# Performance work log

Hardware: AMD Instinct MI355X
Metric: run time of the kernel (lower is better)

## Reference

```python
import jax, jax.numpy as jnp
import numpy as np
from jax import lax

EPS = 1e-8


def setup_inputs() -> dict:
    key = jax.random.key(0)
    k1, k2, k3, k4, k5 = jax.random.split(key, 5)
    b, c_in, c_out, h, w_sp, k, z = 8, 256, 256, 128, 128, 3, 512
    return {
        "x": jax.random.normal(k1, (b, c_in, h, w_sp), dtype=jnp.float32),
        "w": jax.random.normal(k2, (b, z), dtype=jnp.float32),
        "weight": jax.random.normal(k3, (c_out, c_in, k, k), dtype=jnp.float32),
        "affine_w": jax.random.normal(k4, (c_in, z), dtype=jnp.float32) * 0.02,
        "affine_b": jax.random.normal(k5, (c_in,), dtype=jnp.float32) * 0.02,
    }


def reference(x, w, weight, affine_w, affine_b):
    # style: [b, c_in] -> broadcast over (out_ch, kh, kw); +1 as in StyleGAN2
    style = w @ affine_w.T + affine_b + 1.0                      # [b, c_in]
    wgt = weight[None] * style[:, None, :, None, None]           # [b, O, I, kh, kw]
    # demodulation
    denom = lax.rsqrt(jnp.sum(wgt * wgt, axis=(2, 3, 4)) + EPS)  # [b, O]
    wgt = wgt * denom[:, :, None, None, None]

    # per-sample conv (equivalent to groups=b grouped conv), 'same' padding
    def conv_one(xi, wi):
        # xi: [I, H, W], wi: [O, I, kh, kw]
        return lax.conv_general_dilated(
            xi[None], wi, window_strides=(1, 1), padding="SAME",
            dimension_numbers=("NCHW", "OIHW", "NCHW"))[0]

    return jax.vmap(conv_one)(x, wgt)                            # [b, O, H, W]
```

## Files before the change

kernel.cpp:

```cpp
#include <hip/hip_runtime.h>

#define EPS 1e-8f

using short8 = __attribute__((ext_vector_type(8))) short;
using f32x16 = __attribute__((ext_vector_type(16))) float;
typedef unsigned short u16;

#define WAITV(N) asm volatile("s_waitcnt vmcnt(" #N ")" ::: "memory")
#define BARRIER() do { __builtin_amdgcn_s_barrier(); \
                       asm volatile("" ::: "memory"); } while (0)

__device__ __forceinline__ u16 f2bf(float f) {
    union { float f; unsigned u; } v; v.f = f;
    unsigned u = v.u;
    return (u16)((u + 0x7FFFu + ((u >> 16) & 1u)) >> 16);
}

__device__ __forceinline__ void g2l16(const void* gsrc, void* ldst) {
    __builtin_amdgcn_global_load_lds(
        (const __attribute__((address_space(1))) unsigned int*)gsrc,
        (__attribute__((address_space(3))) unsigned int*)ldst, 16, 0, 0);
}

__global__ void style_kernel(const float* __restrict__ w,
                             const float* __restrict__ affine_w,
                             const float* __restrict__ affine_b,
                             float* __restrict__ style) {
    int b = blockIdx.x;
    int i = threadIdx.x;
    __shared__ float wb[512];
    for (int z = threadIdx.x; z < 512; z += 256) wb[z] = w[b * 512 + z];
    __syncthreads();
    const float* aw = affine_w + i * 512;
    float acc = 0.f;
#pragma unroll 4
    for (int z = 0; z < 512; z += 4) {
        float4 a4 = *reinterpret_cast<const float4*>(aw + z);
        acc += a4.x * wb[z] + a4.y * wb[z + 1] + a4.z * wb[z + 2] + a4.w * wb[z + 3];
    }
    style[b * 256 + i] = acc + affine_b[i] + 1.0f;
}

__global__ void modw_kernel(const float* __restrict__ weight,
                            const float* __restrict__ style,
                            u16* __restrict__ wgt) {
    int b = blockIdx.x >> 8;
    int o = blockIdx.x & 255;
    int ic = threadIdx.x;
    float s = style[b * 256 + ic];
    const float* wp = weight + (size_t)(o * 256 + ic) * 9;
    float m[9];
    float ss = 0.f;
#pragma unroll
    for (int t = 0; t < 9; ++t) { m[t] = wp[t] * s; ss += m[t] * m[t]; }
#pragma unroll
    for (int off = 32; off > 0; off >>= 1) ss += __shfl_down(ss, off);
    __shared__ float part[4];
    int lane = threadIdx.x & 63, wid = threadIdx.x >> 6;
    if (lane == 0) part[wid] = ss;
    __syncthreads();
    float denom = rsqrtf(part[0] + part[1] + part[2] + part[3] + EPS);
    int g = ic >> 3, j = ic & 7;
#pragma unroll
    for (int t = 0; t < 9; ++t) {
        size_t idx = ((((size_t)(b * 9 + t) * 32 + g) * 256 + o) << 3) + j;
        wgt[idx] = f2bf(m[t] * denom);
    }
}

__global__ __launch_bounds__(256) void xform_kernel(const float* __restrict__ x,
                                                    u16* __restrict__ xb) {
    int s = blockIdx.x * 256 + threadIdx.x;
    int w = s & 127, h = (s >> 7) & 127, g = (s >> 14) & 31, b = s >> 19;
    const float* xp = x + (((size_t)(b * 256 + g * 8) * 128 + h) * 128 + w);
    union { u16 u[8]; short8 v; } pk;
#pragma unroll
    for (int j = 0; j < 8; ++j) pk.u[j] = f2bf(xp[(size_t)j * 16384]);
    *reinterpret_cast<short8*>(&xb[(size_t)s * 8]) = pk.v;
}

__global__ __launch_bounds__(256, 2) void conv_kernel(
    const u16* __restrict__ xb,
    const u16* __restrict__ wgt,
    float* __restrict__ out) {

    __shared__ __align__(16) u16 Xs[2][4][4][130][8];
    __shared__ __align__(16) u16 trash[1024];

    int bid = blockIdx.x;
    int swz = (bid & 7) * 128 + (bid >> 3);
    int ht = swz & 63, ot = (swz >> 6) & 1, b = swz >> 7;
    int h0 = ht * 2;

    int tid = threadIdx.x, lane = tid & 63, wid = tid >> 6;
    int wm = wid >> 1, wr = wid & 1;
    int l31 = lane & 31, lh = lane >> 5;

    int hr = h0 + wid - 1;
    bool hValid = ((unsigned)hr < 128u);
    int hc = hValid ? hr : 0;

    const u16* aBase = wgt + ((size_t)(b * 9) * 32 * 256 +
                              (size_t)(lh * 256 + ot * 128 + wm * 64 + l31)) * 8;

    auto loadA = [&](short8 dst[2][2], int c, int t) {
#pragma unroll
        for (int kk = 0; kk < 2; ++kk)
#pragma unroll
            for (int mi = 0; mi < 2; ++mi)
                dst[kk][mi] = *reinterpret_cast<const short8*>(
                    aBase + (size_t)(((t * 32) + c * 4 + kk * 2) * 256 + mi * 32) * 8);
    };
    auto stageX = [&](int c1, int bx) {
#pragma unroll
        for (int k = 0; k < 8; ++k) {
            int g = k >> 1, half = k & 1;
            const u16* src = xb +
                ((((size_t)(b * 32 + c1 * 4 + g)) * 128 + hc) * 128 + half * 64 + lane) * 8;
            void* dst = hValid ? (void*)&Xs[bx][wid][g][1 + half * 64][0] : (void*)trash;
            g2l16(src, dst);
        }
    };

    {
        short8 z = {0, 0, 0, 0, 0, 0, 0, 0};
        short8* p0 = reinterpret_cast<short8*>(&Xs[0][0][0][0][0]);
        for (int i = tid; i < 4160; i += 256) p0[i] = z;
    }
    __syncthreads();

    short8 afC[2][2], afN[2][2];
    stageX(0, 0);
    loadA(afC, 0, 0);
    WAITV(4);
    BARRIER();

    f32x16 acc[2][4] = {};

    for (int c = 0; c < 8; ++c) {
        int buf = c & 1;
#pragma unroll
        for (int t = 0; t < 9; ++t) {
            if (!(c == 7 && t == 8))
                loadA(afN, t < 8 ? c : c + 1, t < 8 ? t + 1 : 0);
            if (t == 0 && c < 7) stageX(c + 1, buf ^ 1);

            int kh = t / 3, kw = t - kh * 3;
            short8 bx8[2][4];
#pragma unroll
            for (int kk = 0; kk < 2; ++kk)
#pragma unroll
                for (int ni = 0; ni < 4; ++ni)
                    bx8[kk][ni] = *reinterpret_cast<const short8*>(
                        &Xs[buf][wr + kh][kk * 2 + lh][ni * 32 + l31 + kw][0]);
            __builtin_amdgcn_s_setprio(1);
#pragma unroll
            for (int mi = 0; mi < 2; ++mi)
#pragma unroll
                for (int ni = 0; ni < 4; ++ni)
#pragma unroll
                    for (int kk = 0; kk < 2; ++kk)
                        acc[mi][ni] = __builtin_amdgcn_mfma_f32_32x32x16_bf16(
                            afC[kk][mi], bx8[kk][ni], acc[mi][ni], 0, 0, 0);
            __builtin_amdgcn_s_setprio(0);
#pragma unroll
            for (int kk = 0; kk < 2; ++kk)
#pragma unroll
                for (int mi = 0; mi < 2; ++mi)
                    afC[kk][mi] = afN[kk][mi];
        }
        WAITV(4);
        BARRIER();
    }

    int h = h0 + wr;
#pragma unroll
    for (int mi = 0; mi < 2; ++mi) {
        int ob = ot * 128 + wm * 64 + mi * 32 + 4 * lh;
#pragma unroll
        for (int ni = 0; ni < 4; ++ni) {
            int w_ = ni * 32 + l31;
#pragma unroll
            for (int reg = 0; reg < 16; ++reg) {
                int o = ob + (reg & 3) + 8 * (reg >> 2);
                out[(((size_t)(b * 256 + o) * 128 + h) * 128) + w_] = acc[mi][ni][reg];
            }
        }
    }
}

extern "C" void kernel_launch(void* const* d_in, const int* in_sizes, int n_in,
                              void* d_out, int out_size, void* d_ws, size_t ws_size,
                              hipStream_t stream) {
    const float* x        = (const float*)d_in[0];
    const float* w        = (const float*)d_in[1];
    const float* weight   = (const float*)d_in[2];
    const float* affine_w = (const float*)d_in[3];
    const float* affine_b = (const float*)d_in[4];
    float* out = (float*)d_out;

    float* style = (float*)d_ws;
    u16* wgt = (u16*)((char*)d_ws + 8192);
    u16* xbuf = (u16*)((char*)d_ws + 8192 + 9437184);

    xform_kernel<<<16384, 256, 0, stream>>>(x, xbuf);
    style_kernel<<<8, 256, 0, stream>>>(w, affine_w, affine_b, style);
    modw_kernel<<<2048, 256, 0, stream>>>(weight, style, wgt);
    conv_kernel<<<1024, 256, 0, stream>>>(xbuf, wgt, out);
}
```

Measured before the change: 196.3 us.

## Triple-buffer weight fragments in conv and merge prep kernels into one launch

The conv kernel now keeps three sets of A (weight) fragments and prefetches two taps ahead instead of one, which removes the per-tap register copy. The end-of-chunk wait is relaxed so it only waits for the X staging loads, and it is skipped on the last chunk. Separately, the weight-modulation and x-to-bf16 transform kernels are fused into one launch by splitting on block index, saving a launch. The deeper prefetch raises VGPR pressure under the 2-waves-per-SIMD launch bound.

```diff
diff --git a/kernel.cpp b/kernel.cpp
--- a/kernel.cpp
+++ b/kernel.cpp
@@ -41,42 +41,45 @@
     style[b * 256 + i] = acc + affine_b[i] + 1.0f;
 }
 
-__global__ void modw_kernel(const float* __restrict__ weight,
-                            const float* __restrict__ style,
-                            u16* __restrict__ wgt) {
-    int b = blockIdx.x >> 8;
-    int o = blockIdx.x & 255;
-    int ic = threadIdx.x;
-    float s = style[b * 256 + ic];
-    const float* wp = weight + (size_t)(o * 256 + ic) * 9;
-    float m[9];
-    float ss = 0.f;
-#pragma unroll
-    for (int t = 0; t < 9; ++t) { m[t] = wp[t] * s; ss += m[t] * m[t]; }
-#pragma unroll
-    for (int off = 32; off > 0; off >>= 1) ss += __shfl_down(ss, off);
-    __shared__ float part[4];
-    int lane = threadIdx.x & 63, wid = threadIdx.x >> 6;
-    if (lane == 0) part[wid] = ss;
-    __syncthreads();
-    float denom = rsqrtf(part[0] + part[1] + part[2] + part[3] + EPS);
-    int g = ic >> 3, j = ic & 7;
-#pragma unroll
-    for (int t = 0; t < 9; ++t) {
-        size_t idx = ((((size_t)(b * 9 + t) * 32 + g) * 256 + o) << 3) + j;
-        wgt[idx] = f2bf(m[t] * denom);
-    }
-}
-
-__global__ __launch_bounds__(256) void xform_kernel(const float* __restrict__ x,
-                                                    u16* __restrict__ xb) {
-    int s = blockIdx.x * 256 + threadIdx.x;
-    int w = s & 127, h = (s >> 7) & 127, g = (s >> 14) & 31, b = s >> 19;
-    const float* xp = x + (((size_t)(b * 256 + g * 8) * 128 + h) * 128 + w);
-    union { u16 u[8]; short8 v; } pk;
-#pragma unroll
-    for (int j = 0; j < 8; ++j) pk.u[j] = f2bf(xp[(size_t)j * 16384]);
-    *reinterpret_cast<short8*>(&xb[(size_t)s * 8]) = pk.v;
+__global__ __launch_bounds__(256) void prep_kernel(
+    const float* __restrict__ weight,
+    const float* __restrict__ style,
+    u16* __restrict__ wgt,
+    const float* __restrict__ x,
+    u16* __restrict__ xb) {
+    int blk = blockIdx.x;
+    if (blk < 2048) {
+        int b = blk >> 8;
+        int o = blk & 255;
+        int ic = threadIdx.x;
+        float s = style[b * 256 + ic];
+        const float* wp = weight + (size_t)(o * 256 + ic) * 9;
+        float m[9];
+        float ss = 0.f;
+#pragma unroll
+        for (int t = 0; t < 9; ++t) { m[t] = wp[t] * s; ss += m[t] * m[t]; }
+#pragma unroll
+        for (int off = 32; off > 0; off >>= 1) ss += __shfl_down(ss, off);
+        __shared__ float part[4];
+        int lane = threadIdx.x & 63, wid = threadIdx.x >> 6;
+        if (lane == 0) part[wid] = ss;
+        __syncthreads();
+        float denom = rsqrtf(part[0] + part[1] + part[2] + part[3] + EPS);
+        int g = ic >> 3, j = ic & 7;
+#pragma unroll
+        for (int t = 0; t < 9; ++t) {
+            size_t idx = ((((size_t)(b * 9 + t) * 32 + g) * 256 + o) << 3) + j;
+            wgt[idx] = f2bf(m[t] * denom);
+        }
+    } else {
+        int s = (blk - 2048) * 256 + threadIdx.x;
+        int w = s & 127, h = (s >> 7) & 127, g = (s >> 14) & 31, b = s >> 19;
+        const float* xp = x + (((size_t)(b * 256 + g * 8) * 128 + h) * 128 + w);
+        union { u16 u[8]; short8 v; } pk;
+#pragma unroll
+        for (int j = 0; j < 8; ++j) pk.u[j] = f2bf(xp[(size_t)j * 16384]);
+        *reinterpret_cast<short8*>(&xb[(size_t)s * 8]) = pk.v;
+    }
 }
 
 __global__ __launch_bounds__(256, 2) void conv_kernel(
@@ -129,10 +132,11 @@
     }
     __syncthreads();
 
-    short8 afC[2][2], afN[2][2];
+    short8 af[3][2][2];
     stageX(0, 0);
-    loadA(afC, 0, 0);
-    WAITV(4);
+    loadA(af[0], 0, 0);
+    loadA(af[1], 0, 1);
+    WAITV(8);
     BARRIER();
 
     f32x16 acc[2][4] = {};
@@ -141,8 +145,11 @@
         int buf = c & 1;
 #pragma unroll
         for (int t = 0; t < 9; ++t) {
-            if (!(c == 7 && t == 8))
-                loadA(afN, t < 8 ? c : c + 1, t < 8 ? t + 1 : 0);
+            if (!(c == 7 && t >= 7)) {
+                int tt = t + 2, nc = c, nt = tt;
+                if (tt > 8) { nc = c + 1; nt = tt - 9; }
+                loadA(af[(t + 2) % 3], nc, nt);
+            }
             if (t == 0 && c < 7) stageX(c + 1, buf ^ 1);
 
             int kh = t / 3, kw = t - kh * 3;
@@ -161,16 +168,10 @@
 #pragma unroll
                     for (int kk = 0; kk < 2; ++kk)
                         acc[mi][ni] = __builtin_amdgcn_mfma_f32_32x32x16_bf16(
-                            afC[kk][mi], bx8[kk][ni], acc[mi][ni], 0, 0, 0);
+                            af[t % 3][kk][mi], bx8[kk][ni], acc[mi][ni], 0, 0, 0);
             __builtin_amdgcn_s_setprio(0);
-#pragma unroll
-            for (int kk = 0; kk < 2; ++kk)
-#pragma unroll
-                for (int mi = 0; mi < 2; ++mi)
-                    afC[kk][mi] = afN[kk][mi];
-        }
-        WAITV(4);
-        BARRIER();
+        }
+        if (c < 7) { WAITV(32); BARRIER(); }
     }
 
     int h = h0 + wr;
@@ -203,8 +204,7 @@
     u16* wgt = (u16*)((char*)d_ws + 8192);
     u16* xbuf = (u16*)((char*)d_ws + 8192 + 9437184);
 
-    xform_kernel<<<16384, 256, 0, stream>>>(x, xbuf);
     style_kernel<<<8, 256, 0, stream>>>(w, affine_w, affine_b, style);
-    modw_kernel<<<2048, 256, 0, stream>>>(weight, style, wgt);
+    prep_kernel<<<18432, 256, 0, stream>>>(weight, style, wgt, x, xbuf);
     conv_kernel<<<1024, 256, 0, stream>>>(xbuf, wgt, out);
 }
```

Result: no change. 194.6 us (-0.8%).
